# Kernel optimization log

Hardware: AMD Instinct MI355X
Metric: run time of the kernel (lower is better)

## Reference

```python
import jax, jax.numpy as jnp
import numpy as np

K = 9          # temporal window (kernel_size)
PAD = (K - 1) // 2
BN_EPS = 1e-5


def setup_inputs() -> dict:
    key = jax.random.key(0)
    ks = jax.random.split(key, 9)
    N, Cin, Cout, T, V = 16, 64, 128, 256, 25
    return {
        "x": jax.random.normal(ks[0], (N, Cin, T, V), jnp.float32),
        "conv_w": jax.random.normal(ks[1], (Cout, Cin), jnp.float32) * (1.0 / np.sqrt(Cin)),
        "conv_b": jax.random.normal(ks[2], (Cout,), jnp.float32) * 0.01,
        "gamma": jax.random.uniform(ks[3], (Cout,), jnp.float32, 0.5, 1.5),
        "beta": jax.random.normal(ks[4], (Cout,), jnp.float32) * 0.1,
        "run_mean": jax.random.normal(ks[5], (Cout,), jnp.float32) * 0.1,
        "run_var": jax.random.uniform(ks[6], (Cout,), jnp.float32, 0.5, 1.5),
        "att0": jnp.full((1, Cout, 1, K), 1.0 / K, jnp.float32),
        "A": jax.random.uniform(ks[7], (V, V), jnp.float32),
        "keep_prob": 1,
    }


def reference(x, conv_w, conv_b, gamma, beta, run_mean, run_var, att0, A, keep_prob):
    # 1x1 conv (pointwise channel mix); AvgPool2d((1,1)) is identity for stride=1
    x = jnp.einsum("nctv,oc->notv", x, conv_w) + conv_b[None, :, None, None]
    # BatchNorm2d (eval mode: running stats)
    scale = gamma / jnp.sqrt(run_var + BN_EPS)
    x = x * scale[None, :, None, None] + (beta - run_mean * scale)[None, :, None, None]
    N, C, T, V = x.shape
    # UnfoldTemporalWindows: zero-pad T, gather K temporal shifts -> (N, C, T, K, V)
    xp = jnp.pad(x, ((0, 0), (0, 0), (PAD, PAD), (0, 0)))
    upfold = jnp.stack([xp[:, :, u:u + T, :] for u in range(K)], axis=3)
    # local attention: score each window position against the center frame
    scores = jnp.einsum("nctv,nctuv->nctu", x, upfold) / V
    attn = jax.nn.softmax(scores, axis=-1) + att0
    out = jnp.einsum("nctuv,nctu->nctv", upfold, attn)
    # dropS / dropT are identity at keep_prob == 1 (inference)
    return out
```

## Files before the change

kernel.cpp:

```cpp
#include <hip/hip_runtime.h>
#include <hip/hip_bf16.h>

#define CIN   64
#define COUT  128
#define TT    256
#define VV    25
#define TV    (TT * VV)
#define KW    9
#define PAD   4
#define YROW  28
#define YSTR  (TT * YROW)

typedef __attribute__((ext_vector_type(8))) short short8;
typedef __attribute__((ext_vector_type(4))) float f32x4;

__device__ __forceinline__ unsigned f2b(float f) {
    unsigned u = __builtin_bit_cast(unsigned, f);
    return (u + 0x7FFFu + ((u >> 16) & 1u)) >> 16;
}
__device__ __forceinline__ float lof(unsigned u) {
    return __builtin_bit_cast(float, u << 16);
}
__device__ __forceinline__ float hif(unsigned u) {
    return __builtin_bit_cast(float, u & 0xffff0000u);
}
__device__ __forceinline__ int swz(int row, int cbyte) {
    return row * 128 + ((cbyte & ~15) ^ ((row & 7) << 4)) + (cbyte & 15);
}

__global__ __launch_bounds__(256) void conv_mfma(
    const float* __restrict__ x, const float* __restrict__ w,
    const float* __restrict__ cb, const float* __restrict__ gamma,
    const float* __restrict__ beta, const float* __restrict__ rm,
    const float* __restrict__ rv, unsigned short* __restrict__ y)
{
    __shared__ __align__(16) unsigned short Wl[COUT * 64];
    __shared__ __align__(16) unsigned short Xl[128 * 64];
    __shared__ float sc[COUT];
    __shared__ float of[COUT];

    const int pc  = blockIdx.x;
    const int n   = blockIdx.y;
    const int tid = threadIdx.x;
    const int posbase = pc * 128;

    if (tid < COUT) {
        const float s = gamma[tid] * rsqrtf(rv[tid] + 1e-5f);
        sc[tid] = s;
        of[tid] = cb[tid] * s + beta[tid] - rm[tid] * s;
    }
    for (int idx = tid; idx < 2048; idx += 256) {
        const int c4 = idx & 15, o = idx >> 4;
        const f32x4 wv = *(const f32x4*)(w + o * 64 + c4 * 4);
        uint2 pk;
        pk.x = f2b(wv.x) | (f2b(wv.y) << 16);
        pk.y = f2b(wv.z) | (f2b(wv.w) << 16);
        *(uint2*)((char*)Wl + swz(o, c4 * 8)) = pk;
    }
    for (int idx = tid; idx < 2048; idx += 256) {
        const int pos = idx & 127, c4 = idx >> 7;
        const float* xp = x + (size_t)n * CIN * TV + (size_t)(c4 * 4) * TV + posbase + pos;
        const float a0 = xp[0], a1 = xp[TV], a2 = xp[2 * TV], a3 = xp[3 * TV];
        uint2 pk;
        pk.x = f2b(a0) | (f2b(a1) << 16);
        pk.y = f2b(a2) | (f2b(a3) << 16);
        *(uint2*)((char*)Xl + swz(pos, c4 * 8)) = pk;
    }
    __syncthreads();

    const int wv_ = tid >> 6, lane = tid & 63;
    const int lr = lane & 15, lh = lane >> 4;

    short8 afr[2][2];
#pragma unroll
    for (int m0 = 0; m0 < 2; ++m0)
#pragma unroll
        for (int kh = 0; kh < 2; ++kh)
            afr[m0][kh] = *(const short8*)((const char*)Wl +
                              swz(wv_ * 32 + m0 * 16 + lr, kh * 64 + lh * 16));

    f32x4 acc[2][8];
#pragma unroll
    for (int m0 = 0; m0 < 2; ++m0)
#pragma unroll
        for (int n0 = 0; n0 < 8; ++n0) acc[m0][n0] = (f32x4){0.f, 0.f, 0.f, 0.f};

#pragma unroll
    for (int n0 = 0; n0 < 8; ++n0) {
        const int prow = n0 * 16 + lr;
        const short8 b0 = *(const short8*)((const char*)Xl + swz(prow, lh * 16));
        const short8 b1 = *(const short8*)((const char*)Xl + swz(prow, 64 + lh * 16));
#pragma unroll
        for (int m0 = 0; m0 < 2; ++m0) {
            acc[m0][n0] = __builtin_amdgcn_mfma_f32_16x16x32_bf16(afr[m0][0], b0, acc[m0][n0], 0, 0, 0);
            acc[m0][n0] = __builtin_amdgcn_mfma_f32_16x16x32_bf16(afr[m0][1], b1, acc[m0][n0], 0, 0, 0);
        }
    }

    float scv[2][4], ofv[2][4];
#pragma unroll
    for (int m0 = 0; m0 < 2; ++m0)
#pragma unroll
        for (int r = 0; r < 4; ++r) {
            const int o = wv_ * 32 + m0 * 16 + lh * 4 + r;
            scv[m0][r] = sc[o];
            ofv[m0][r] = of[o];
        }

    const size_t ybase = (size_t)(n * COUT) * YSTR;
#pragma unroll
    for (int m0 = 0; m0 < 2; ++m0)
#pragma unroll
        for (int n0 = 0; n0 < 8; ++n0)
#pragma unroll
            for (int r = 0; r < 4; ++r) {
                const int o = wv_ * 32 + m0 * 16 + lh * 4 + r;
                const int pos = posbase + n0 * 16 + lr;
                const int t = pos / 25;
                const int v = pos - t * 25;
                const float val = acc[m0][n0][r] * scv[m0][r] + ofv[m0][r];
                y[ybase + (size_t)o * YSTR + t * YROW + v] = (unsigned short)f2b(val);
            }
}

#define UC(u,cc) ((cc)==0?(u).x:((cc)==1?(u).y:((cc)==2?(u).z:(u).w)))
#define DW(k) ((k)<4?UC(u0_,(k)):((k)<8?UC(u1_,(k)-4):((k)<12?UC(u2_,(k)-8):UC(u3_,(k)-12))))
#define LOADROW(rl, par, dst)                                               \
    {                                                                       \
        const int ub_ = (7 * (rl) - (par)) >> 1;                            \
        const uint4 u0_ = tl[ub_], u1_ = tl[ub_ + 1];                       \
        const uint4 u2_ = tl[ub_ + 2], u3_ = tl[ub_ + 3];                   \
        _Pragma("unroll")                                                   \
        for (int v_ = 0; v_ < 25; ++v_) {                                   \
            const int k_ = 2 * (par) + (v_ >> 1);                           \
            const unsigned dw_ = DW(k_);                                    \
            (dst)[v_] = (v_ & 1) ? hif(dw_) : lof(dw_);                     \
        }                                                                   \
    }

__global__ __launch_bounds__(128) void attn_kernel(
    const unsigned short* __restrict__ y, const float* __restrict__ att0,
    float* __restrict__ out)
{
    __shared__ __align__(16) float sm[TV];
    __shared__ float a0s[KW];

    uint4* tl = (uint4*)sm;

    const int nc  = blockIdx.x;
    const int c   = nc & (COUT - 1);
    const int tid = threadIdx.x;

    if (tid < KW) a0s[tid] = att0[c * KW + tid];

    if (tid < 28) {
        const int i = (tid < 14) ? tid : (896 + tid);
        tl[i] = make_uint4(0, 0, 0, 0);
    }
    const uint4* yg = (const uint4*)(y + (size_t)nc * YSTR);
#pragma unroll
    for (int i = 0; i < 7; ++i) tl[14 + tid + i * 128] = yg[tid + i * 128];
    __syncthreads();

    const int t0 = tid * 2;

    float q0[25], q1[25];
    LOADROW(t0 + 4, 0, q0);
    LOADROW(t0 + 5, 1, q1);

    float s0[KW], s1[KW];
    {
        float a0_ = 0.f, a1_ = 0.f, b0_ = 0.f, b1_ = 0.f, c0_ = 0.f, c1_ = 0.f;
#pragma unroll
        for (int v = 0; v < 12; ++v) {
            a0_ = fmaf(q0[v], q0[v], a0_);
            b0_ = fmaf(q0[v], q1[v], b0_);
            c0_ = fmaf(q1[v], q1[v], c0_);
        }
#pragma unroll
        for (int v = 12; v < 25; ++v) {
            a1_ = fmaf(q0[v], q0[v], a1_);
            b1_ = fmaf(q0[v], q1[v], b1_);
            c1_ = fmaf(q1[v], q1[v], c1_);
        }
        s0[4] = (a0_ + a1_) * (1.f / 25.f);
        s0[5] = (b0_ + b1_) * (1.f / 25.f);
        s1[3] = s0[5];
        s1[4] = (c0_ + c1_) * (1.f / 25.f);
    }

#pragma unroll
    for (int j = 0; j < 10; ++j) {
        if (j == 4 || j == 5) continue;
        float row[25];
        LOADROW(t0 + j, (j & 1), row);
        float d0a = 0.f, d0b = 0.f, d1a = 0.f, d1b = 0.f;
#pragma unroll
        for (int v = 0; v < 12; ++v) {
            d0a = fmaf(row[v], q0[v], d0a);
            d1a = fmaf(row[v], q1[v], d1a);
        }
#pragma unroll
        for (int v = 12; v < 25; ++v) {
            d0b = fmaf(row[v], q0[v], d0b);
            d1b = fmaf(row[v], q1[v], d1b);
        }
        if (j <= 8) s0[j]     = (d0a + d0b) * (1.f / 25.f);
        if (j >= 1) s1[j - 1] = (d1a + d1b) * (1.f / 25.f);
    }

    {
        float m0 = s0[0], m1 = s1[0];
#pragma unroll
        for (int u = 1; u < KW; ++u) { m0 = fmaxf(m0, s0[u]); m1 = fmaxf(m1, s1[u]); }
        float d0 = 0.f, d1 = 0.f;
#pragma unroll
        for (int u = 0; u < KW; ++u) {
            s0[u] = __expf(s0[u] - m0); d0 += s0[u];
            s1[u] = __expf(s1[u] - m1); d1 += s1[u];
        }
        const float i0 = 1.f / d0, i1 = 1.f / d1;
#pragma unroll
        for (int u = 0; u < KW; ++u) {
            s0[u] = s0[u] * i0 + a0s[u];
            s1[u] = s1[u] * i1 + a0s[u];
        }
    }

    float o0[25], o1[25];
#pragma unroll
    for (int v = 0; v < 25; ++v) {
        o0[v] = s0[4] * q0[v] + s0[5] * q1[v];
        o1[v] = s1[3] * q0[v] + s1[4] * q1[v];
    }
#pragma unroll
    for (int j = 0; j < 10; ++j) {
        if (j == 4 || j == 5) continue;
        float row[25];
        LOADROW(t0 + j, (j & 1), row);
        if (j <= 8) {
            const float a = s0[j];
#pragma unroll
            for (int v = 0; v < 25; ++v) o0[v] = fmaf(a, row[v], o0[v]);
        }
        if (j >= 1) {
            const float a = s1[j - 1];
#pragma unroll
            for (int v = 0; v < 25; ++v) o1[v] = fmaf(a, row[v], o1[v]);
        }
    }

    __syncthreads();
    {
        float* dst = &sm[t0 * 25];
#pragma unroll
        for (int k = 0; k < 25; ++k) {
            const int j0 = 2 * k, j1 = 2 * k + 1;
            const float a = (j0 < 25) ? o0[j0] : o1[j0 - 25];
            const float b = (j1 < 25) ? o0[j1] : o1[j1 - 25];
            *(float2*)(dst + j0) = make_float2(a, b);
        }
    }
    __syncthreads();

    {
        float4* og = (float4*)(out + (size_t)nc * TV);
        const float4* sm4 = (const float4*)sm;
        for (int i = tid; i < TV / 4; i += 128) og[i] = sm4[i];
    }
}

extern "C" void kernel_launch(void* const* d_in, const int* in_sizes, int n_in,
                              void* d_out, int out_size, void* d_ws, size_t ws_size,
                              hipStream_t stream)
{
    const float* x     = (const float*)d_in[0];
    const float* w     = (const float*)d_in[1];
    const float* cb    = (const float*)d_in[2];
    const float* gamma = (const float*)d_in[3];
    const float* beta  = (const float*)d_in[4];
    const float* rm    = (const float*)d_in[5];
    const float* rv    = (const float*)d_in[6];
    const float* att0  = (const float*)d_in[7];
    float* out = (float*)d_out;
    unsigned short* y = (unsigned short*)d_ws;

    dim3 gA(TV / 128, 16);
    conv_mfma<<<gA, 256, 0, stream>>>(x, w, cb, gamma, beta, rm, rv, y);

    dim3 gB(16 * COUT);
    attn_kernel<<<gB, 128, 0, stream>>>(y, att0, out);
}
```

Before: 48.08 us.

## Use one thread per time step with single-pass unnormalized softmax in attention

The attention kernel now launches 256 threads per block, one per time step, instead of 128 threads each handling two steps. Each thread accumulates exp-weighted and att0-weighted outputs in a single pass over the window rows, dropping the separate score pass and the max subtraction. The parity of each step is made warp-uniform through a templated core. This raises parallelism and removes re-reading rows from LDS, at the cost of losing row sharing between adjacent steps and dropping the max-stabilised softmax, which risks overflow for large scores.

```diff
diff --git a/kernel.cpp b/kernel.cpp
--- a/kernel.cpp
+++ b/kernel.cpp
@@ -138,7 +138,54 @@
         }                                                                   \
     }
 
-__global__ __launch_bounds__(128) void attn_kernel(
+template<int PAR>
+__device__ __forceinline__ void attn_core(const uint4* tl, const float* a0s,
+                                          int t, float* outv)
+{
+    float q[25];
+    LOADROW(t + 4, PAR, q);
+
+    float osm[25], oa0[25];
+    float den;
+    {
+        float d0 = 0.f, d1 = 0.f;
+#pragma unroll
+        for (int v = 0; v < 12; ++v)  d0 = fmaf(q[v], q[v], d0);
+#pragma unroll
+        for (int v = 12; v < 25; ++v) d1 = fmaf(q[v], q[v], d1);
+        const float e = __expf((d0 + d1) * (1.f / 25.f));
+        den = e;
+        const float a = a0s[4];
+#pragma unroll
+        for (int v = 0; v < 25; ++v) { osm[v] = e * q[v]; oa0[v] = a * q[v]; }
+    }
+
+#pragma unroll
+    for (int j = 0; j < KW; ++j) {
+        if (j == 4) continue;
+        float row[25];
+        LOADROW(t + j, PAR ^ (j & 1), row);
+        float d0 = 0.f, d1 = 0.f;
+#pragma unroll
+        for (int v = 0; v < 12; ++v)  d0 = fmaf(row[v], q[v], d0);
+#pragma unroll
+        for (int v = 12; v < 25; ++v) d1 = fmaf(row[v], q[v], d1);
+        const float e = __expf((d0 + d1) * (1.f / 25.f));
+        den += e;
+        const float a = a0s[j];
+#pragma unroll
+        for (int v = 0; v < 25; ++v) {
+            osm[v] = fmaf(e, row[v], osm[v]);
+            oa0[v] = fmaf(a, row[v], oa0[v]);
+        }
+    }
+
+    const float inv = 1.f / den;
+#pragma unroll
+    for (int v = 0; v < 25; ++v) outv[v] = fmaf(osm[v], inv, oa0[v]);
+}
+
+__global__ __launch_bounds__(256) void attn_kernel(
     const unsigned short* __restrict__ y, const float* __restrict__ att0,
     float* __restrict__ out)
 {
@@ -159,114 +206,36 @@
     }
     const uint4* yg = (const uint4*)(y + (size_t)nc * YSTR);
 #pragma unroll
-    for (int i = 0; i < 7; ++i) tl[14 + tid + i * 128] = yg[tid + i * 128];
-    __syncthreads();
-
-    const int t0 = tid * 2;
-
-    float q0[25], q1[25];
-    LOADROW(t0 + 4, 0, q0);
-    LOADROW(t0 + 5, 1, q1);
-
-    float s0[KW], s1[KW];
+    for (int i = 0; i < 4; ++i) {
+        const int ci = tid + i * 256;
+        if (ci < 896) tl[14 + ci] = yg[ci];
+    }
+    __syncthreads();
+
+    const int w   = tid >> 6;
+    const int par = (w >> 1) & 1;
+    const int t   = ((w & 1) << 7) + ((tid & 63) << 1) + par;
+
+    float outv[25];
+    if (par == 0) attn_core<0>(tl, a0s, t, outv);
+    else          attn_core<1>(tl, a0s, t, outv);
+
+    __syncthreads();
     {
-        float a0_ = 0.f, a1_ = 0.f, b0_ = 0.f, b1_ = 0.f, c0_ = 0.f, c1_ = 0.f;
-#pragma unroll
-        for (int v = 0; v < 12; ++v) {
-            a0_ = fmaf(q0[v], q0[v], a0_);
-            b0_ = fmaf(q0[v], q1[v], b0_);
-            c0_ = fmaf(q1[v], q1[v], c0_);
-        }
-#pragma unroll
-        for (int v = 12; v < 25; ++v) {
-            a1_ = fmaf(q0[v], q0[v], a1_);
-            b1_ = fmaf(q0[v], q1[v], b1_);
-            c1_ = fmaf(q1[v], q1[v], c1_);
-        }
-        s0[4] = (a0_ + a1_) * (1.f / 25.f);
-        s0[5] = (b0_ + b1_) * (1.f / 25.f);
-        s1[3] = s0[5];
-        s1[4] = (c0_ + c1_) * (1.f / 25.f);
-    }
-
-#pragma unroll
-    for (int j = 0; j < 10; ++j) {
-        if (j == 4 || j == 5) continue;
-        float row[25];
-        LOADROW(t0 + j, (j & 1), row);
-        float d0a = 0.f, d0b = 0.f, d1a = 0.f, d1b = 0.f;
-#pragma unroll
-        for (int v = 0; v < 12; ++v) {
-            d0a = fmaf(row[v], q0[v], d0a);
-            d1a = fmaf(row[v], q1[v], d1a);
-        }
-#pragma unroll
-        for (int v = 12; v < 25; ++v) {
-            d0b = fmaf(row[v], q0[v], d0b);
-            d1b = fmaf(row[v], q1[v], d1b);
-        }
-        if (j <= 8) s0[j]     = (d0a + d0b) * (1.f / 25.f);
-        if (j >= 1) s1[j - 1] = (d1a + d1b) * (1.f / 25.f);
-    }
-
-    {
-        float m0 = s0[0], m1 = s1[0];
-#pragma unroll
-        for (int u = 1; u < KW; ++u) { m0 = fmaxf(m0, s0[u]); m1 = fmaxf(m1, s1[u]); }
-        float d0 = 0.f, d1 = 0.f;
-#pragma unroll
-        for (int u = 0; u < KW; ++u) {
-            s0[u] = __expf(s0[u] - m0); d0 += s0[u];
-            s1[u] = __expf(s1[u] - m1); d1 += s1[u];
-        }
-        const float i0 = 1.f / d0, i1 = 1.f / d1;
-#pragma unroll
-        for (int u = 0; u < KW; ++u) {
-            s0[u] = s0[u] * i0 + a0s[u];
-            s1[u] = s1[u] * i1 + a0s[u];
-        }
-    }
-
-    float o0[25], o1[25];
-#pragma unroll
-    for (int v = 0; v < 25; ++v) {
-        o0[v] = s0[4] * q0[v] + s0[5] * q1[v];
-        o1[v] = s1[3] * q0[v] + s1[4] * q1[v];
-    }
-#pragma unroll
-    for (int j = 0; j < 10; ++j) {
-        if (j == 4 || j == 5) continue;
-        float row[25];
-        LOADROW(t0 + j, (j & 1), row);
-        if (j <= 8) {
-            const float a = s0[j];
-#pragma unroll
-            for (int v = 0; v < 25; ++v) o0[v] = fmaf(a, row[v], o0[v]);
-        }
-        if (j >= 1) {
-            const float a = s1[j - 1];
-#pragma unroll
-            for (int v = 0; v < 25; ++v) o1[v] = fmaf(a, row[v], o1[v]);
-        }
-    }
-
-    __syncthreads();
-    {
-        float* dst = &sm[t0 * 25];
-#pragma unroll
-        for (int k = 0; k < 25; ++k) {
-            const int j0 = 2 * k, j1 = 2 * k + 1;
-            const float a = (j0 < 25) ? o0[j0] : o1[j0 - 25];
-            const float b = (j1 < 25) ? o0[j1] : o1[j1 - 25];
-            *(float2*)(dst + j0) = make_float2(a, b);
-        }
+        float* dst = &sm[t * 25];
+#pragma unroll
+        for (int v = 0; v < 25; ++v) dst[v] = outv[v];
     }
     __syncthreads();
 
     {
         float4* og = (float4*)(out + (size_t)nc * TV);
         const float4* sm4 = (const float4*)sm;
-        for (int i = tid; i < TV / 4; i += 128) og[i] = sm4[i];
+#pragma unroll
+        for (int i = 0; i < 7; ++i) {
+            const int ci = tid + i * 256;
+            if (ci < TV / 4) og[ci] = sm4[ci];
+        }
     }
 }
 
@@ -289,5 +258,5 @@
     conv_mfma<<<gA, 256, 0, stream>>>(x, w, cb, gamma, beta, rm, rv, y);
 
     dim3 gB(16 * COUT);
-    attn_kernel<<<gB, 128, 0, stream>>>(y, att0, out);
-}
+    attn_kernel<<<gB, 256, 0, stream>>>(y, att0, out);
+}
```

New measurement: 67.20 us. +39.8%, slower.
